# Optimization experiments

Hardware: AMD Instinct MI355X
Metric: run time of the kernel (lower is better)

The kernel has to match this reference:

```python
import jax, jax.numpy as jnp
import numpy as np

N_NODES = 50000
N_EDGES = 800000
D = 128          # node/edge feature dim
H = 128          # MLP hidden dim
T_EDGE = 3       # number of edge types
T_NODE = 2       # number of node types


def setup_inputs() -> dict:
    key = jax.random.key(0)
    ks = jax.random.split(key, 14)
    s = 0.05  # weight init scale
    return {
        "nf": jax.random.normal(ks[0], (N_NODES, D), jnp.float32),
        "ef": jax.random.normal(ks[1], (N_EDGES, D), jnp.float32),
        "src": jax.random.randint(ks[2], (N_EDGES,), 0, N_NODES, jnp.int32),
        "dst": jax.random.randint(ks[3], (N_EDGES,), 0, N_NODES, jnp.int32),
        "etype": jax.random.randint(ks[4], (N_EDGES,), 0, T_EDGE, jnp.int32),
        "ntype": jax.random.randint(ks[5], (N_NODES,), 0, T_NODE, jnp.int32),
        # per-edge-type MLP: Linear(3D->H), ReLU, Linear(H->D)
        "We_h": jax.random.normal(ks[6], (T_EDGE, 3 * D, H), jnp.float32) * s,
        "be_h": jnp.zeros((T_EDGE, H), jnp.float32),
        "We_o": jax.random.normal(ks[7], (T_EDGE, H, D), jnp.float32) * s,
        "be_o": jnp.zeros((T_EDGE, D), jnp.float32),
        # per-node-type MLP: Linear(2D->H), ReLU, Linear(H->D)
        "Wn_h": jax.random.normal(ks[8], (T_NODE, 2 * D, H), jnp.float32) * s,
        "bn_h": jnp.zeros((T_NODE, H), jnp.float32),
        "Wn_o": jax.random.normal(ks[9], (T_NODE, H, D), jnp.float32) * s,
        "bn_o": jnp.zeros((T_NODE, D), jnp.float32),
    }


def _typed_mlp(x, tvec, Wh, bh, Wo, bo):
    """Per-type 2-layer MLP dispatch, then the source's gather-back.

    The torch code builds type_pos_list (stable concat of per-type index lists,
    i.e. a stable argsort of tvec) and then indexes the concatenated per-type
    outputs with that same permutation (`updated[type_perm]`, a gather rather
    than an inverse-permutation scatter). We reproduce that exactly:
    out_final[j] = out_correct[perm[perm[j]]].
    """
    T = Wh.shape[0]
    out = jnp.zeros((x.shape[0], Wo.shape[-1]), x.dtype)
    for k in range(T):  # small fixed number of types
        y = jax.nn.relu(x @ Wh[k] + bh[k]) @ Wo[k] + bo[k]
        out = jnp.where((tvec == k)[:, None], y, out)
    perm = jnp.argsort(tvec)  # jax argsort is stable
    return out[perm[perm]]


def reference(nf, ef, src, dst, etype, ntype,
              We_h, be_h, We_o, be_o, Wn_h, bn_h, Wn_o, bn_o):
    # edge update: cat([ef, src_nf, dst_nf]) -> per-type MLP
    em_in = jnp.concatenate([ef, nf[src], nf[dst]], axis=-1)  # [E, 3D]
    new_ef = _typed_mlp(em_in, etype, We_h, be_h, We_o, be_o)  # [E, D]
    # message passing: copy_e('h') messages, sum reduce into dst nodes
    agg_m = jax.ops.segment_sum(new_ef, dst, num_segments=nf.shape[0])  # [N, D]
    # node update: cat([agg_m, nf]) -> per-type MLP
    nm_in = jnp.concatenate([agg_m, nf], axis=-1)  # [N, 2D]
    new_nf = _typed_mlp(nm_in, ntype, Wn_h, bn_h, Wn_o, bn_o)  # [N, D]
    return new_nf, new_ef
```

## Files before the change

kernel.cpp:

```cpp
#include <hip/hip_runtime.h>

typedef __bf16 bf16_t;
typedef bf16_t bf16x2_t __attribute__((ext_vector_type(2)));
typedef bf16_t bf16x8_t __attribute__((ext_vector_type(8)));
typedef float  f32x4_t  __attribute__((ext_vector_type(4)));

#define RCHUNK 4096
#define MFMA16(a, b, c) __builtin_amdgcn_mfma_f32_16x16x32_bf16((a), (b), (c), 0, 0, 0)

__global__ void pack_w_kernel(const float* __restrict__ W, bf16_t* __restrict__ out,
                              int T, int Ksrc, int k0, int KB)
{
  int total = T * KB * 8 * 512;
  for (int idx = blockIdx.x * blockDim.x + threadIdx.x; idx < total;
       idx += gridDim.x * blockDim.x) {
    int j  = idx & 7;
    int l  = (idx >> 3) & 63;
    int nb = (idx >> 9) & 7;
    int r  = idx >> 12;
    int kb = r % KB;
    int t  = r / KB;
    int k = k0 + kb * 32 + ((l >> 4) << 3) + j;
    int n = nb * 16 + (l & 15);
    out[idx] = (bf16_t)W[((size_t)t * Ksrc + k) * 128 + n];
  }
}

template <int T>
__global__ void count_types_kernel(const int* __restrict__ tv, int n,
                                   int* __restrict__ blkcnt)
{
  __shared__ int cnt[T];
  int tid = threadIdx.x, b = blockIdx.x;
  if (tid < T) cnt[tid] = 0;
  __syncthreads();
  int lo = b * RCHUNK, hi = min(n, lo + RCHUNK);
  int loc[T];
#pragma unroll
  for (int t = 0; t < T; ++t) loc[t] = 0;
  for (int i = lo + tid; i < hi; i += 256) {
    int tq = tv[i];
#pragma unroll
    for (int t = 0; t < T; ++t) loc[t] += (tq == t);
  }
#pragma unroll
  for (int t = 0; t < T; ++t)
    if (loc[t]) atomicAdd(&cnt[t], loc[t]);
  __syncthreads();
  if (tid < T) blkcnt[b * T + tid] = cnt[tid];
}

template <int T>
__global__ void scan_blocks_kernel(const int* __restrict__ blkcnt, int nblocks,
                                   int* __restrict__ blkbase)
{
  __shared__ int sh[256];
  __shared__ int tot[T];
  int tid = threadIdx.x;
  int myc[T], excl[T];
#pragma unroll
  for (int t = 0; t < T; ++t) myc[t] = (tid < nblocks) ? blkcnt[tid * T + t] : 0;
#pragma unroll
  for (int t = 0; t < T; ++t) {
    sh[tid] = myc[t];
    __syncthreads();
    for (int off = 1; off < 256; off <<= 1) {
      int v = (tid >= off) ? sh[tid - off] : 0;
      __syncthreads();
      sh[tid] += v;
      __syncthreads();
    }
    excl[t] = sh[tid] - myc[t];
    if (tid == 255) tot[t] = sh[255];
    __syncthreads();
  }
  if (tid < nblocks) {
    int run = 0;
#pragma unroll
    for (int t = 0; t < T; ++t) {
      blkbase[tid * T + t] = run + excl[t];
      run += tot[t];
    }
  }
}

template <int T>
__global__ void write_ranks_kernel(const int* __restrict__ tv, int n,
                                   const int* __restrict__ blkbase,
                                   int* __restrict__ rank, int* __restrict__ perm)
{
  __shared__ int sh[256];
  int tid = threadIdx.x, b = blockIdx.x;
  int lo = b * RCHUNK + tid * 16;
  int tvq[16];
  int myc[T];
#pragma unroll
  for (int t = 0; t < T; ++t) myc[t] = 0;
#pragma unroll
  for (int q = 0; q < 16; ++q) {
    int i = lo + q;
    int tq = (i < n) ? tv[i] : -1;
    tvq[q] = tq;
#pragma unroll
    for (int t = 0; t < T; ++t) myc[t] += (tq == t);
  }
  int mybase[T];
#pragma unroll
  for (int t = 0; t < T; ++t) {
    sh[tid] = myc[t];
    __syncthreads();
    for (int off = 1; off < 256; off <<= 1) {
      int v = (tid >= off) ? sh[tid - off] : 0;
      __syncthreads();
      sh[tid] += v;
      __syncthreads();
    }
    mybase[t] = blkbase[b * T + t] + sh[tid] - myc[t];
    __syncthreads();
  }
#pragma unroll
  for (int q = 0; q < 16; ++q) {
    int tq = tvq[q];
    if (tq < 0) continue;
    int r = 0;
#pragma unroll
    for (int t = 0; t < T; ++t)
      if (tq == t) { r = mybase[t]; mybase[t] = r + 1; }
    rank[lo + q] = r;
    perm[r] = lo + q;
  }
}

__global__ void key_hist_kernel(const int* __restrict__ rank,
                                const int* __restrict__ dst,
                                const int* __restrict__ tb, int E, int Nn,
                                int* __restrict__ key, int* __restrict__ khist)
{
  int pos = blockIdx.x * blockDim.x + threadIdx.x;
  if (pos < E) {
    int t = (pos >= tb[1]) + (pos >= tb[2]);
    int k = t * Nn + dst[rank[pos]];
    key[pos] = k;
    atomicAdd(&khist[k], 1);
  }
}

__global__ __launch_bounds__(1024) void mscan_pass1(const int* __restrict__ h,
                                                    int n, int* __restrict__ part)
{
  __shared__ int sh[1024];
  int tid = threadIdx.x;
  int i0 = blockIdx.x * 4096 + tid * 4;
  int s = 0;
#pragma unroll
  for (int q = 0; q < 4; ++q) { int i = i0 + q; s += (i < n) ? h[i] : 0; }
  sh[tid] = s;
  __syncthreads();
  for (int off = 512; off > 0; off >>= 1) {
    if (tid < off) sh[tid] += sh[tid + off];
    __syncthreads();
  }
  if (tid == 0) part[blockIdx.x] = sh[0];
}

__global__ __launch_bounds__(1024) void mscan_pass2(int* __restrict__ part, int nb)
{
  __shared__ int sh[1024];
  int tid = threadIdx.x;
  int v = (tid < nb) ? part[tid] : 0;
  sh[tid] = v;
  __syncthreads();
  for (int off = 1; off < 1024; off <<= 1) {
    int u = (tid >= off) ? sh[tid - off] : 0;
    __syncthreads();
    sh[tid] += u;
    __syncthreads();
  }
  if (tid < nb) part[tid] = sh[tid] - v;
  if (tid == 1023) part[nb] = sh[1023];
}

__global__ __launch_bounds__(1024) void mscan_pass3(
    const int* __restrict__ h, int n, const int* __restrict__ part, int nb,
    int* __restrict__ offs, int* __restrict__ cur)
{
  __shared__ int sh[1024];
  int tid = threadIdx.x;
  int i0 = blockIdx.x * 4096 + tid * 4;
  int v[4];
  int s = 0;
#pragma unroll
  for (int q = 0; q < 4; ++q) { int i = i0 + q; v[q] = (i < n) ? h[i] : 0; s += v[q]; }
  sh[tid] = s;
  __syncthreads();
  for (int off = 1; off < 1024; off <<= 1) {
    int u = (tid >= off) ? sh[tid - off] : 0;
    __syncthreads();
    sh[tid] += u;
    __syncthreads();
  }
  int run = part[blockIdx.x] + sh[tid] - s;
#pragma unroll
  for (int q = 0; q < 4; ++q) {
    int i = i0 + q;
    if (i < n) { offs[i] = run; cur[i] = run; run += v[q]; }
  }
  if (blockIdx.x == 0 && tid == 0) offs[n] = part[nb];
}

__global__ void build_meta_slot_kernel(const int* __restrict__ key,
                                       const int* __restrict__ perm,
                                       const int* __restrict__ rank,
                                       const int* __restrict__ src,
                                       const int* __restrict__ dst,
                                       int* __restrict__ kcursor,
                                       int4* __restrict__ meta4,
                                       int* __restrict__ jmap, int E)
{
  int pos = blockIdx.x * blockDim.x + threadIdx.x;
  if (pos < E) {
    int slot = atomicAdd(&kcursor[key[pos]], 1);
    int e = perm[pos];
    int j = rank[pos];
    int4 m;
    m.x = e; m.y = src[e]; m.z = dst[e]; m.w = j;
    meta4[slot] = m;
    jmap[slot] = j;
  }
}

__global__ void gather_meta_node_kernel(const int* __restrict__ perm,
                                        const int* __restrict__ rank,
                                        int4* __restrict__ meta4, int N)
{
  int i = blockIdx.x * blockDim.x + threadIdx.x;
  if (i < N) {
    int e = perm[i];
    int4 m;
    m.x = e; m.y = e; m.z = e; m.w = rank[i];
    meta4[i] = m;
  }
}

__global__ __launch_bounds__(256) void aggregate_scatter_kernel(
    const bf16_t* __restrict__ slot_buf, const int* __restrict__ koffs,
    const int* __restrict__ jmap, float* __restrict__ out_ef,
    float* __restrict__ agg, int Nn)
{
  int gw = (blockIdx.x * 256 + threadIdx.x) >> 6;
  int l = threadIdx.x & 63;
  int nw = (gridDim.x * 256) >> 6;
  for (int n = gw; n < Nn; n += nw) {
    float sx = 0.f, sy = 0.f;
#pragma unroll
    for (int t = 0; t < 3; ++t) {
      int k = t * Nn + n;
      int lo = koffs[k], hi = koffs[k + 1];
      int q = lo;
      for (; q + 1 < hi; q += 2) {
        bf16x2_t v0 = *(const bf16x2_t*)(slot_buf + (size_t)q * 128 + l * 2);
        bf16x2_t v1 = *(const bf16x2_t*)(slot_buf + (size_t)(q + 1) * 128 + l * 2);
        int j0 = jmap[q], j1 = jmap[q + 1];
        float a0 = (float)v0[0], a1 = (float)v0[1];
        float b0 = (float)v1[0], b1 = (float)v1[1];
        sx += a0 + b0; sy += a1 + b1;
        float2 o0; o0.x = a0; o0.y = a1;
        float2 o1; o1.x = b0; o1.y = b1;
        *(float2*)(out_ef + (size_t)j0 * 128 + l * 2) = o0;
        *(float2*)(out_ef + (size_t)j1 * 128 + l * 2) = o1;
      }
      if (q < hi) {
        bf16x2_t v0 = *(const bf16x2_t*)(slot_buf + (size_t)q * 128 + l * 2);
        int j0 = jmap[q];
        float a0 = (float)v0[0], a1 = (float)v0[1];
        sx += a0; sy += a1;
        float2 o0; o0.x = a0; o0.y = a1;
        *(float2*)(out_ef + (size_t)j0 * 128 + l * 2) = o0;
      }
    }
    float2 o; o.x = sx; o.y = sy;
    *(float2*)(agg + (size_t)n * 128 + l * 2) = o;
  }
}

__global__ __launch_bounds__(256, 4) void precompute_p2_kernel(
    const float* __restrict__ nf,
    const bf16_t* __restrict__ pW1s, const bf16_t* __restrict__ pW1d,
    const bf16_t* __restrict__ pWn1b,
    bf16_t* __restrict__ Ps, bf16_t* __restrict__ Pd, bf16_t* __restrict__ Pn,
    int Nn)
{
  __shared__ char Ysm[16384];
  const int tid = threadIdx.x, l = tid & 63, w = tid >> 6;
  const int rb = (w >> 1) * 32, cb = (w & 1) * 64, l15 = l & 15;
  const int koff = (l >> 4) << 3;
  const int base = blockIdx.x * 64;

  const int r0 = min(base + rb + l15, Nn - 1);
  const int r1 = min(base + rb + l15 + 16, Nn - 1);
  const float* q0 = nf + (size_t)r0 * 128 + koff;
  const float* q1 = nf + (size_t)r1 * 128 + koff;
  bf16x8_t a0[4], a1[4];
#pragma unroll
  for (int kb = 0; kb < 4; ++kb) {
    f32x4_t u0 = ((const f32x4_t*)(q0 + kb * 32))[0];
    f32x4_t u1 = ((const f32x4_t*)(q0 + kb * 32))[1];
    f32x4_t u2 = ((const f32x4_t*)(q1 + kb * 32))[0];
    f32x4_t u3 = ((const f32x4_t*)(q1 + kb * 32))[1];
#pragma unroll
    for (int z = 0; z < 4; ++z) {
      a0[kb][z] = (bf16_t)u0[z]; a0[kb][4 + z] = (bf16_t)u1[z];
      a1[kb][z] = (bf16_t)u2[z]; a1[kb][4 + z] = (bf16_t)u3[z];
    }
  }

  for (int which = 0; which < 8; ++which) {
    const bf16_t* pB; bf16_t* po;
    if (which < 3)      { pB = pW1s + which * 16384;        po = Ps + (size_t)which * Nn * 128; }
    else if (which < 6) { pB = pW1d + (which - 3) * 16384;  po = Pd + (size_t)(which - 3) * Nn * 128; }
    else                { pB = pWn1b + (which - 6) * 16384; po = Pn + (size_t)(which - 6) * Nn * 128; }
    const bf16x8_t* wg = (const bf16x8_t*)pB;

    f32x4_t acc[2][4];
#pragma unroll
    for (int m = 0; m < 2; ++m)
#pragma unroll
      for (int n = 0; n < 4; ++n) acc[m][n] = (f32x4_t){0.f, 0.f, 0.f, 0.f};
#pragma unroll
    for (int kb = 0; kb < 4; ++kb) {
      bf16x8_t bfr[4];
#pragma unroll
      for (int n = 0; n < 4; ++n)
        bfr[n] = wg[(size_t)((kb * 8 + (cb >> 4) + n) * 64 + l)];
#pragma unroll
      for (int n = 0; n < 4; ++n) {
        acc[0][n] = MFMA16(a0[kb], bfr[n], acc[0][n]);
        acc[1][n] = MFMA16(a1[kb], bfr[n], acc[1][n]);
      }
    }

    __syncthreads();
#pragma unroll
    for (int n = 0; n < 4; ++n) {
      int col = cb + 16 * n + l15;
#pragma unroll
      for (int m = 0; m < 2; ++m)
#pragma unroll
        for (int jj = 0; jj < 4; ++jj) {
          int row = rb + 16 * m + ((l >> 4) << 2) + jj;
          *(bf16_t*)(Ysm + row * 256 + ((col * 2) ^ ((row & 7) << 4))) =
              (bf16_t)acc[m][n][jj];
        }
    }
    __syncthreads();
    {
      int row = tid >> 2, cpart = tid & 3;
      int node = base + row;
      if (node < Nn) {
        bf16_t* dstp = po + (size_t)node * 128 + cpart * 32;
#pragma unroll
        for (int q = 0; q < 4; ++q) {
          int c = cpart * 4 + q;
          *(uint4*)(dstp + q * 8) = *(const uint4*)(
              Ysm + row * 256 + ((c * 16) ^ ((row & 7) << 4)));
        }
      }
    }
  }
}

template <int T, bool EDGE>
__global__ __launch_bounds__(256, 3) void mlp9_kernel(
    const float* __restrict__ feat,
    const int4* __restrict__ meta4,
    const int* __restrict__ tbase,
    const bf16_t* __restrict__ pW1, const float* __restrict__ b1,
    const bf16_t* __restrict__ pW2, const float* __restrict__ b2,
    const bf16_t* __restrict__ P1, const bf16_t* __restrict__ P2, int pnodes,
    float* __restrict__ out, bf16_t* __restrict__ slot_out, int Ntot)
{
  __shared__ char Wsm[32768];
  __shared__ char Hsm[16384];
  __shared__ int sm_e[64], sm_sl[64], sm_s0[64], sm_s1[64];

  const int tid = threadIdx.x;
  const int l = tid & 63, w = tid >> 6;
  const int rb = (w >> 1) * 32, cb = (w & 1) * 64;
  const int l15 = l & 15;
  const int koff = (l >> 4) << 3;

  const int s0 = tbase[0];
  const int s1 = (T > 1) ? tbase[1] : Ntot;
  const int s2 = (T > 2) ? tbase[2] : Ntot;
  const int e0t = (T > 1) ? s1 : Ntot;
  const int e1t = (T > 2) ? s2 : Ntot;
  const int c0 = (e0t - s0 + 63) >> 6;
  const int c1 = (T > 1) ? ((e1t - s1 + 63) >> 6) : 0;
  const int c2 = (T > 2) ? ((Ntot - s2 + 63) >> 6) : 0;
  const int cum1 = c0, cum2 = c0 + c1, total = cum2 + c2;

  const int tpb = (total + gridDim.x - 1) / gridDim.x;
  const int pt0 = blockIdx.x * tpb;
  const int pt1 = min(total, pt0 + tpb);

  int cur_t = -1;
  bf16x8_t w2r[16];
  float bh[4], bo[4];

  for (int pt = pt0; pt < pt1; ++pt) {
    const int t = (pt < cum1) ? 0 : ((pt < cum2) ? 1 : 2);
    const int tstart = (t == 0) ? s0 : ((t == 1) ? s1 : s2);
    const int tend = (t == 0) ? e0t : ((t == 1) ? e1t : Ntot);
    const int i = pt - ((t == 0) ? 0 : ((t == 1) ? cum1 : cum2));
    const int pbase = tstart + (i << 6);

    __syncthreads();
    if (tid < 64) {
      int pos = pbase + tid;
      if (pos < tend) {
        int4 m = meta4[pos];
        sm_e[tid] = m.x;
        sm_sl[tid] = m.w;
        if (EDGE) { sm_s0[tid] = m.y; sm_s1[tid] = m.z; }
      } else {
        sm_e[tid] = 0; sm_sl[tid] = -1;
        if (EDGE) { sm_s0[tid] = 0; sm_s1[tid] = 0; }
      }
    }
    __syncthreads();

    const int ar0 = rb + l15, ar1 = ar0 + 16;
    const float* q0 = feat + (size_t)sm_e[ar0] * 128 + koff;
    const float* q1 = feat + (size_t)sm_e[ar1] * 128 + koff;
    f32x4_t areg[2][4][2];
#pragma unroll
    for (int kb = 0; kb < 4; ++kb) {
      areg[0][kb][0] = ((const f32x4_t*)(q0 + kb * 32))[0];
      areg[0][kb][1] = ((const f32x4_t*)(q0 + kb * 32))[1];
      areg[1][kb][0] = ((const f32x4_t*)(q1 + kb * 32))[0];
      areg[1][kb][1] = ((const f32x4_t*)(q1 + kb * 32))[1];
    }

#pragma unroll
    for (int q = 0; q < 4; ++q) {
      int idx = tid * 4 + q;
      int row = idx >> 4, c8 = idx & 15;
      bf16x8_t s;
      if (EDGE) {
        bf16x8_t u = ((const bf16x8_t*)(P1 + ((size_t)t * pnodes + sm_s0[row]) * 128))[c8];
        bf16x8_t v = ((const bf16x8_t*)(P2 + ((size_t)t * pnodes + sm_s1[row]) * 128))[c8];
#pragma unroll
        for (int z = 0; z < 8; ++z) s[z] = (bf16_t)((float)u[z] + (float)v[z]);
      } else {
        s = ((const bf16x8_t*)(P1 + ((size_t)t * pnodes + sm_e[row]) * 128))[c8];
      }
      *(bf16x8_t*)(Hsm + row * 256 + ((c8 << 4) ^ ((row & 7) << 4))) = s;
    }

    if (t != cur_t) {
      __syncthreads();
      {
        const uint4* g = (const uint4*)(pW1 + (size_t)t * 16384);
        uint4* d = (uint4*)Wsm;
#pragma unroll
        for (int q = 0; q < 8; ++q) d[q * 256 + tid] = g[q * 256 + tid];
      }
      {
        const bf16x8_t* g2 = (const bf16x8_t*)pW2;
#pragma unroll
        for (int kb = 0; kb < 4; ++kb)
#pragma unroll
          for (int n = 0; n < 4; ++n)
            w2r[kb * 4 + n] = g2[(size_t)((t * 4 + kb) * 8 + (cb >> 4) + n) * 64 + l];
      }
#pragma unroll
      for (int n = 0; n < 4; ++n) {
        bh[n] = b1[t * 128 + cb + 16 * n + l15];
        bo[n] = b2[t * 128 + cb + 16 * n + l15];
      }
      cur_t = t;
      __syncthreads();
    }

    f32x4_t acc[2][4];
#pragma unroll
    for (int m = 0; m < 2; ++m)
#pragma unroll
      for (int n = 0; n < 4; ++n) acc[m][n] = (f32x4_t){0.f, 0.f, 0.f, 0.f};

#pragma unroll
    for (int kb = 0; kb < 4; ++kb) {
      bf16x8_t bfr[4];
#pragma unroll
      for (int n = 0; n < 4; ++n)
        bfr[n] = *(const bf16x8_t*)(Wsm + ((kb * 8 + (cb >> 4) + n) * 64 + l) * 16);
      bf16x8_t a0, a1;
#pragma unroll
      for (int z = 0; z < 4; ++z) {
        a0[z] = (bf16_t)areg[0][kb][0][z]; a0[4 + z] = (bf16_t)areg[0][kb][1][z];
        a1[z] = (bf16_t)areg[1][kb][0][z]; a1[4 + z] = (bf16_t)areg[1][kb][1][z];
      }
#pragma unroll
      for (int n = 0; n < 4; ++n) {
        acc[0][n] = MFMA16(a0, bfr[n], acc[0][n]);
        acc[1][n] = MFMA16(a1, bfr[n], acc[1][n]);
      }
    }

    __syncthreads();
#pragma unroll
    for (int n = 0; n < 4; ++n) {
      int col = cb + 16 * n + l15;
      int byte = col * 2;
#pragma unroll
      for (int m = 0; m < 2; ++m)
#pragma unroll
        for (int jj = 0; jj < 4; ++jj) {
          int row = rb + 16 * m + ((l >> 4) << 2) + jj;
          char* addr = Hsm + row * 256 + (byte ^ ((row & 7) << 4));
          float pv = (float)*(const bf16_t*)addr;
          float v = acc[m][n][jj] + pv + bh[n];
          v = v > 0.f ? v : 0.f;
          *(bf16_t*)addr = (bf16_t)v;
        }
    }
    __syncthreads();

    f32x4_t acc2[2][4];
#pragma unroll
    for (int m = 0; m < 2; ++m)
#pragma unroll
      for (int n = 0; n < 4; ++n) acc2[m][n] = (f32x4_t){0.f, 0.f, 0.f, 0.f};

#pragma unroll
    for (int kb = 0; kb < 4; ++kb) {
      int kbyte = kb * 64 + ((l >> 4) << 4);
      int row0 = rb + l15, row1 = row0 + 16;
      bf16x8_t h0 = *(const bf16x8_t*)(Hsm + row0 * 256 + (kbyte ^ ((row0 & 7) << 4)));
      bf16x8_t h1 = *(const bf16x8_t*)(Hsm + row1 * 256 + (kbyte ^ ((row1 & 7) << 4)));
#pragma unroll
      for (int n = 0; n < 4; ++n) {
        acc2[0][n] = MFMA16(h0, w2r[kb * 4 + n], acc2[0][n]);
        acc2[1][n] = MFMA16(h1, w2r[kb * 4 + n], acc2[1][n]);
      }
    }

    if (EDGE) {
      __syncthreads();
#pragma unroll
      for (int n = 0; n < 4; ++n) {
        int col = cb + 16 * n + l15;
#pragma unroll
        for (int m = 0; m < 2; ++m)
#pragma unroll
          for (int jj = 0; jj < 4; ++jj) {
            int row = rb + 16 * m + ((l >> 4) << 2) + jj;
            *(bf16_t*)(Hsm + row * 256 + ((col * 2) ^ ((row & 7) << 4))) =
                (bf16_t)(acc2[m][n][jj] + bo[n]);
          }
      }
      __syncthreads();
      {
        int row = tid >> 2, cpart = tid & 3;
        if (sm_sl[row] >= 0) {
          char* dstp = (char*)slot_out + (size_t)(pbase + row) * 256 + cpart * 64;
#pragma unroll
          for (int q = 0; q < 4; ++q) {
            int c = cpart * 4 + q;
            *(uint4*)(dstp + q * 16) = *(const uint4*)(
                Hsm + row * 256 + ((c * 16) ^ ((row & 7) << 4)));
          }
        }
      }
    } else {
#pragma unroll
      for (int n = 0; n < 4; ++n) {
        int col = cb + 16 * n + l15;
#pragma unroll
        for (int m = 0; m < 2; ++m)
#pragma unroll
          for (int jj = 0; jj < 4; ++jj) {
            int row = rb + 16 * m + ((l >> 4) << 2) + jj;
            int j = sm_sl[row];
            if (j >= 0) out[(size_t)j * 128 + col] = acc2[m][n][jj] + bo[n];
          }
      }
    }
  }
}

extern "C" void kernel_launch(void* const* d_in, const int* in_sizes, int n_in,
                              void* d_out, int out_size, void* d_ws, size_t ws_size,
                              hipStream_t stream)
{
  const float* nf    = (const float*)d_in[0];
  const float* ef    = (const float*)d_in[1];
  const int*   src   = (const int*)d_in[2];
  const int*   dst   = (const int*)d_in[3];
  const int*   etype = (const int*)d_in[4];
  const int*   ntype = (const int*)d_in[5];
  const float* Weh   = (const float*)d_in[6];
  const float* beh   = (const float*)d_in[7];
  const float* Weo   = (const float*)d_in[8];
  const float* beo   = (const float*)d_in[9];
  const float* Wnh   = (const float*)d_in[10];
  const float* bnh   = (const float*)d_in[11];
  const float* Wno   = (const float*)d_in[12];
  const float* bno   = (const float*)d_in[13];

  const int E = in_sizes[2];
  const int N = in_sizes[5];
  const int TE = 3, TN = 2;

  char* ws = (char*)d_ws;
  size_t off = 0;
  auto alloc = [&](size_t bytes) -> char* {
    char* p = ws + off;
    off = (off + bytes + 511) & ~(size_t)511;
    return p;
  };
  bf16_t* pW1e  = (bf16_t*)alloc((size_t)TE * 16384 * 2);
  bf16_t* pW1s  = (bf16_t*)alloc((size_t)TE * 16384 * 2);
  bf16_t* pW1d  = (bf16_t*)alloc((size_t)TE * 16384 * 2);
  bf16_t* pWe2  = (bf16_t*)alloc((size_t)TE * 16384 * 2);
  bf16_t* pWn1a = (bf16_t*)alloc((size_t)TN * 16384 * 2);
  bf16_t* pWn1b = (bf16_t*)alloc((size_t)TN * 16384 * 2);
  bf16_t* pWn2  = (bf16_t*)alloc((size_t)TN * 16384 * 2);
  bf16_t* Ps = (bf16_t*)alloc((size_t)TE * N * 128 * 2);
  bf16_t* Pd = (bf16_t*)alloc((size_t)TE * N * 128 * 2);
  bf16_t* Pn = (bf16_t*)alloc((size_t)TN * N * 128 * 2);
  int* rank_e = (int*)alloc((size_t)E * 4);
  int* perm_e = (int*)alloc((size_t)E * 4);
  int* rank_n = (int*)alloc((size_t)N * 4);
  int* perm_n = (int*)alloc((size_t)N * 4);
  const int NBE = (E + RCHUNK - 1) / RCHUNK;
  const int NBN = (N + RCHUNK - 1) / RCHUNK;
  int* blkcnt_e  = (int*)alloc((size_t)NBE * TE * 4);
  int* blkbase_e = (int*)alloc((size_t)NBE * TE * 4);
  int* blkcnt_n  = (int*)alloc((size_t)NBN * TN * 4);
  int* blkbase_n = (int*)alloc((size_t)NBN * TN * 4);
  float* agg = (float*)alloc((size_t)N * 128 * 4);
  const int NK = TE * N;
  const int NSB = (NK + 4095) / 4096;
  int* key     = (int*)alloc((size_t)E * 4);
  int* khist   = (int*)alloc((size_t)NK * 4);
  int* koffs   = (int*)alloc((size_t)(NK + 1) * 4);
  int* kcursor = (int*)alloc((size_t)NK * 4);
  int* kpart   = (int*)alloc((size_t)(NSB + 1) * 4);
  int* jmap    = (int*)alloc((size_t)E * 4);
  int4* meta4_e = (int4*)alloc((size_t)E * 16);
  int4* meta4_n = (int4*)alloc((size_t)N * 16);
  bf16_t* slot_buf = (bf16_t*)alloc((size_t)E * 128 * 2);
  (void)ws_size; (void)n_in; (void)out_size;

  pack_w_kernel<<<192, 256, 0, stream>>>(Weh, pW1e, TE, 384, 0, 4);
  pack_w_kernel<<<192, 256, 0, stream>>>(Weh, pW1s, TE, 384, 128, 4);
  pack_w_kernel<<<192, 256, 0, stream>>>(Weh, pW1d, TE, 384, 256, 4);
  pack_w_kernel<<<192, 256, 0, stream>>>(Weo, pWe2, TE, 128, 0, 4);
  pack_w_kernel<<<128, 256, 0, stream>>>(Wnh, pWn1a, TN, 256, 0, 4);
  pack_w_kernel<<<128, 256, 0, stream>>>(Wnh, pWn1b, TN, 256, 128, 4);
  pack_w_kernel<<<128, 256, 0, stream>>>(Wno, pWn2, TN, 128, 0, 4);

  const int ptiles = (N + 63) / 64;
  precompute_p2_kernel<<<ptiles, 256, 0, stream>>>(
      nf, pW1s, pW1d, pWn1b, Ps, Pd, Pn, N);

  count_types_kernel<3><<<NBE, 256, 0, stream>>>(etype, E, blkcnt_e);
  scan_blocks_kernel<3><<<1, 256, 0, stream>>>(blkcnt_e, NBE, blkbase_e);
  write_ranks_kernel<3><<<NBE, 256, 0, stream>>>(etype, E, blkbase_e, rank_e, perm_e);

  count_types_kernel<2><<<NBN, 256, 0, stream>>>(ntype, N, blkcnt_n);
  scan_blocks_kernel<2><<<1, 256, 0, stream>>>(blkcnt_n, NBN, blkbase_n);
  write_ranks_kernel<2><<<NBN, 256, 0, stream>>>(ntype, N, blkbase_n, rank_n, perm_n);

  hipMemsetAsync(khist, 0, (size_t)NK * 4, stream);
  key_hist_kernel<<<(E + 255) / 256, 256, 0, stream>>>(
      rank_e, dst, blkbase_e, E, N, key, khist);
  mscan_pass1<<<NSB, 1024, 0, stream>>>(khist, NK, kpart);
  mscan_pass2<<<1, 1024, 0, stream>>>(kpart, NSB);
  mscan_pass3<<<NSB, 1024, 0, stream>>>(khist, NK, kpart, NSB, koffs, kcursor);
  build_meta_slot_kernel<<<(E + 255) / 256, 256, 0, stream>>>(
      key, perm_e, rank_e, src, dst, kcursor, meta4_e, jmap, E);

  gather_meta_node_kernel<<<(N + 255) / 256, 256, 0, stream>>>(
      perm_n, rank_n, meta4_n, N);

  float* out_nf = (float*)d_out;
  float* out_ef = (float*)d_out + (size_t)N * 128;

  mlp9_kernel<3, true><<<768, 256, 0, stream>>>(
      ef, meta4_e, blkbase_e,
      pW1e, beh, pWe2, beo, Ps, Pd, N, nullptr, slot_buf, E);

  aggregate_scatter_kernel<<<3200, 256, 0, stream>>>(
      slot_buf, koffs, jmap, out_ef, agg, N);

  mlp9_kernel<2, false><<<768, 256, 0, stream>>>(
      agg, meta4_n, blkbase_n,
      pWn1a, bnh, pWn2, bno, Pn, nullptr, N, out_nf, nullptr, N);
}
```

Measured before the change: 776.7 us.

## Fuse edge output scatter and dst aggregation into edge MLP epilogue with atomics

The edge MLP kernel now writes its fp32 output straight to the final gathered positions and accumulates per-destination sums into agg with run-length-merged float atomics. This removes the bf16 slot buffer round trip and the separate aggregate_scatter kernel. It adds a memset of agg, atomic contention on agg, and nondeterministic summation order. Sorting by key still groups each destination within a tile, which limits how many atomics are issued.

```diff
diff --git a/kernel.cpp b/kernel.cpp
--- a/kernel.cpp
+++ b/kernel.cpp
@@ -215,7 +215,7 @@
                                        const int* __restrict__ dst,
                                        int* __restrict__ kcursor,
                                        int4* __restrict__ meta4,
-                                       int* __restrict__ jmap, int E)
+                                       int* __restrict__ dstj, int E)
 {
   int pos = blockIdx.x * blockDim.x + threadIdx.x;
   if (pos < E) {
@@ -225,7 +225,7 @@
     int4 m;
     m.x = e; m.y = src[e]; m.z = dst[e]; m.w = j;
     meta4[slot] = m;
-    jmap[slot] = j;
+    dstj[slot] = dst[j];
   }
 }
 
@@ -242,47 +242,6 @@
   }
 }
 
-__global__ __launch_bounds__(256) void aggregate_scatter_kernel(
-    const bf16_t* __restrict__ slot_buf, const int* __restrict__ koffs,
-    const int* __restrict__ jmap, float* __restrict__ out_ef,
-    float* __restrict__ agg, int Nn)
-{
-  int gw = (blockIdx.x * 256 + threadIdx.x) >> 6;
-  int l = threadIdx.x & 63;
-  int nw = (gridDim.x * 256) >> 6;
-  for (int n = gw; n < Nn; n += nw) {
-    float sx = 0.f, sy = 0.f;
-#pragma unroll
-    for (int t = 0; t < 3; ++t) {
-      int k = t * Nn + n;
-      int lo = koffs[k], hi = koffs[k + 1];
-      int q = lo;
-      for (; q + 1 < hi; q += 2) {
-        bf16x2_t v0 = *(const bf16x2_t*)(slot_buf + (size_t)q * 128 + l * 2);
-        bf16x2_t v1 = *(const bf16x2_t*)(slot_buf + (size_t)(q + 1) * 128 + l * 2);
-        int j0 = jmap[q], j1 = jmap[q + 1];
-        float a0 = (float)v0[0], a1 = (float)v0[1];
-        float b0 = (float)v1[0], b1 = (float)v1[1];
-        sx += a0 + b0; sy += a1 + b1;
-        float2 o0; o0.x = a0; o0.y = a1;
-        float2 o1; o1.x = b0; o1.y = b1;
-        *(float2*)(out_ef + (size_t)j0 * 128 + l * 2) = o0;
-        *(float2*)(out_ef + (size_t)j1 * 128 + l * 2) = o1;
-      }
-      if (q < hi) {
-        bf16x2_t v0 = *(const bf16x2_t*)(slot_buf + (size_t)q * 128 + l * 2);
-        int j0 = jmap[q];
-        float a0 = (float)v0[0], a1 = (float)v0[1];
-        sx += a0; sy += a1;
-        float2 o0; o0.x = a0; o0.y = a1;
-        *(float2*)(out_ef + (size_t)j0 * 128 + l * 2) = o0;
-      }
-    }
-    float2 o; o.x = sx; o.y = sy;
-    *(float2*)(agg + (size_t)n * 128 + l * 2) = o;
-  }
-}
-
 __global__ __launch_bounds__(256, 4) void precompute_p2_kernel(
     const float* __restrict__ nf,
     const bf16_t* __restrict__ pW1s, const bf16_t* __restrict__ pW1d,
@@ -370,18 +329,19 @@
 }
 
 template <int T, bool EDGE>
-__global__ __launch_bounds__(256, 3) void mlp9_kernel(
+__global__ __launch_bounds__(256, 3) void mlp10_kernel(
     const float* __restrict__ feat,
     const int4* __restrict__ meta4,
+    const int* __restrict__ dstj,
     const int* __restrict__ tbase,
     const bf16_t* __restrict__ pW1, const float* __restrict__ b1,
     const bf16_t* __restrict__ pW2, const float* __restrict__ b2,
     const bf16_t* __restrict__ P1, const bf16_t* __restrict__ P2, int pnodes,
-    float* __restrict__ out, bf16_t* __restrict__ slot_out, int Ntot)
+    float* __restrict__ out, float* __restrict__ agg_out, int Ntot)
 {
   __shared__ char Wsm[32768];
   __shared__ char Hsm[16384];
-  __shared__ int sm_e[64], sm_sl[64], sm_s0[64], sm_s1[64];
+  __shared__ int sm_e[64], sm_sl[64], sm_s0[64], sm_s1[64], sm_key[64];
 
   const int tid = threadIdx.x;
   const int l = tid & 63, w = tid >> 6;
@@ -421,10 +381,10 @@
         int4 m = meta4[pos];
         sm_e[tid] = m.x;
         sm_sl[tid] = m.w;
-        if (EDGE) { sm_s0[tid] = m.y; sm_s1[tid] = m.z; }
+        if (EDGE) { sm_s0[tid] = m.y; sm_s1[tid] = m.z; sm_key[tid] = dstj[pos]; }
       } else {
         sm_e[tid] = 0; sm_sl[tid] = -1;
-        if (EDGE) { sm_s0[tid] = 0; sm_s1[tid] = 0; }
+        if (EDGE) { sm_s0[tid] = 0; sm_s1[tid] = 0; sm_key[tid] = -1; }
       }
     }
     __syncthreads();
@@ -545,6 +505,19 @@
       }
     }
 
+#pragma unroll
+    for (int n = 0; n < 4; ++n) {
+      int col = cb + 16 * n + l15;
+#pragma unroll
+      for (int m = 0; m < 2; ++m)
+#pragma unroll
+        for (int jj = 0; jj < 4; ++jj) {
+          int row = rb + 16 * m + ((l >> 4) << 2) + jj;
+          int j = sm_sl[row];
+          if (j >= 0) out[(size_t)j * 128 + col] = acc2[m][n][jj] + bo[n];
+        }
+    }
+
     if (EDGE) {
       __syncthreads();
 #pragma unroll
@@ -561,29 +534,25 @@
       }
       __syncthreads();
       {
-        int row = tid >> 2, cpart = tid & 3;
-        if (sm_sl[row] >= 0) {
-          char* dstp = (char*)slot_out + (size_t)(pbase + row) * 256 + cpart * 64;
-#pragma unroll
-          for (int q = 0; q < 4; ++q) {
-            int c = cpart * 4 + q;
-            *(uint4*)(dstp + q * 16) = *(const uint4*)(
-                Hsm + row * 256 + ((c * 16) ^ ((row & 7) << 4)));
+        int c = tid & 127, h = tid >> 7;
+        int byte = c * 2;
+        int cur = -1;
+        float s = 0.f;
+#pragma unroll 8
+        for (int r = 0; r < 32; ++r) {
+          int row = (h << 5) + r;
+          int k = sm_key[row];
+          if (k != cur) {
+            if (cur >= 0)
+              unsafeAtomicAdd(agg_out + (size_t)cur * 128 + c, s);
+            s = 0.f;
+            cur = k;
           }
+          if (k >= 0)
+            s += (float)*(const bf16_t*)(Hsm + row * 256 + (byte ^ ((row & 7) << 4)));
         }
-      }
-    } else {
-#pragma unroll
-      for (int n = 0; n < 4; ++n) {
-        int col = cb + 16 * n + l15;
-#pragma unroll
-        for (int m = 0; m < 2; ++m)
-#pragma unroll
-          for (int jj = 0; jj < 4; ++jj) {
-            int row = rb + 16 * m + ((l >> 4) << 2) + jj;
-            int j = sm_sl[row];
-            if (j >= 0) out[(size_t)j * 128 + col] = acc2[m][n][jj] + bo[n];
-          }
+        if (cur >= 0)
+          unsafeAtomicAdd(agg_out + (size_t)cur * 128 + c, s);
       }
     }
   }
@@ -647,10 +616,9 @@
   int* koffs   = (int*)alloc((size_t)(NK + 1) * 4);
   int* kcursor = (int*)alloc((size_t)NK * 4);
   int* kpart   = (int*)alloc((size_t)(NSB + 1) * 4);
-  int* jmap    = (int*)alloc((size_t)E * 4);
+  int* dstj    = (int*)alloc((size_t)E * 4);
   int4* meta4_e = (int4*)alloc((size_t)E * 16);
   int4* meta4_n = (int4*)alloc((size_t)N * 16);
-  bf16_t* slot_buf = (bf16_t*)alloc((size_t)E * 128 * 2);
   (void)ws_size; (void)n_in; (void)out_size;
 
   pack_w_kernel<<<192, 256, 0, stream>>>(Weh, pW1e, TE, 384, 0, 4);
@@ -680,7 +648,7 @@
   mscan_pass2<<<1, 1024, 0, stream>>>(kpart, NSB);
   mscan_pass3<<<NSB, 1024, 0, stream>>>(khist, NK, kpart, NSB, koffs, kcursor);
   build_meta_slot_kernel<<<(E + 255) / 256, 256, 0, stream>>>(
-      key, perm_e, rank_e, src, dst, kcursor, meta4_e, jmap, E);
+      key, perm_e, rank_e, src, dst, kcursor, meta4_e, dstj, E);
 
   gather_meta_node_kernel<<<(N + 255) / 256, 256, 0, stream>>>(
       perm_n, rank_n, meta4_n, N);
@@ -688,14 +656,13 @@
   float* out_nf = (float*)d_out;
   float* out_ef = (float*)d_out + (size_t)N * 128;
 
-  mlp9_kernel<3, true><<<768, 256, 0, stream>>>(
-      ef, meta4_e, blkbase_e,
-      pW1e, beh, pWe2, beo, Ps, Pd, N, nullptr, slot_buf, E);
-
-  aggregate_scatter_kernel<<<3200, 256, 0, stream>>>(
-      slot_buf, koffs, jmap, out_ef, agg, N);
-
-  mlp9_kernel<2, false><<<768, 256, 0, stream>>>(
-      agg, meta4_n, blkbase_n,
+  hipMemsetAsync(agg, 0, (size_t)N * 128 * 4, stream);
+
+  mlp10_kernel<3, true><<<768, 256, 0, stream>>>(
+      ef, meta4_e, dstj, blkbase_e,
+      pW1e, beh, pWe2, beo, Ps, Pd, N, out_ef, agg, E);
+
+  mlp10_kernel<2, false><<<768, 256, 0, stream>>>(
+      agg, meta4_n, nullptr, blkbase_n,
       pWn1a, bnh, pWn2, bno, Pn, nullptr, N, out_nf, nullptr, N);
 }
```

Result: faster. 745.7 us (-4.0%).
